# Kernel optimization log

Measured on AMD Instinct MI355X. Metric: run time of the kernel, lower is better.

The kernel has to match this reference:

```python
import jax, jax.numpy as jnp
import numpy as np

NEG_SLOPE = 0.2  # LeakyReLU slope

N, E, D_IN, D_OUT, H, NBIN = 50000, 500000, 256, 256, 8, 10
DH = D_OUT // H


def setup_inputs() -> dict:
    key = jax.random.key(0)
    ks = jax.random.split(key, 9)
    emb_rel = jax.random.normal(ks[0], (N, D_IN), dtype=jnp.float32)
    head_idxs = jax.random.randint(ks[1], (E,), 0, N, dtype=jnp.int32)
    tail_idxs = jax.random.randint(ks[2], (E,), 0, N, dtype=jnp.int32)
    bins = jax.random.randint(ks[3], (E,), 0, NBIN, dtype=jnp.int32)
    # xavier-normal-ish scaled params (gain for relu)
    attn_proj_w = jax.random.normal(ks[4], (D_OUT, 2 * D_IN), dtype=jnp.float32) * (1.4142 * (2.0 / (2 * D_IN + D_OUT)) ** 0.5)
    attn_proj_b = jnp.zeros((D_OUT,), dtype=jnp.float32)
    attn_bin = jax.random.normal(ks[5], (NBIN, H, 1), dtype=jnp.float32) * 0.3
    attn_vec = jax.random.normal(ks[6], (1, H, DH), dtype=jnp.float32) * (1.4142 * (2.0 / (H + DH)) ** 0.5)
    aggr_proj_w = jax.random.normal(ks[7], (D_OUT, D_IN), dtype=jnp.float32) * (1.4142 * (2.0 / (D_IN + D_OUT)) ** 0.5)
    aggr_proj_b = jnp.zeros((D_OUT,), dtype=jnp.float32)
    return {
        "emb_rel": emb_rel,
        "head_idxs": head_idxs,
        "tail_idxs": tail_idxs,
        "bins": bins,
        "attn_proj_w": attn_proj_w,
        "attn_proj_b": attn_proj_b,
        "attn_bin": attn_bin,
        "attn_vec": attn_vec,
        "aggr_proj_w": aggr_proj_w,
        "aggr_proj_b": aggr_proj_b,
        "num_nodes": N,
    }


def reference(emb_rel, head_idxs, tail_idxs, bins, attn_proj_w, attn_proj_b,
              attn_bin, attn_vec, aggr_proj_w, aggr_proj_b, num_nodes):
    num_head, dim_hid = attn_vec.shape[1], attn_vec.shape[2]
    eh = emb_rel[head_idxs]                      # (E, D_in)
    et = emb_rel[tail_idxs]                      # (E, D_in)
    concat = jnp.concatenate([eh, et], axis=-1)  # (E, 2*D_in)
    proj = (concat @ attn_proj_w.T + attn_proj_b).reshape(-1, num_head, dim_hid)
    lrelu = jnp.where(proj >= 0, proj, NEG_SLOPE * proj)
    # raw attention logits per edge/head: (E, H, 1)
    attn_raw = jnp.sum(lrelu * attn_vec, axis=-1, keepdims=True) + attn_bin[bins]
    # segmented softmax over edges grouped by head node
    seg_max = jax.ops.segment_max(attn_raw, head_idxs, num_segments=num_nodes)
    seg_max = jnp.where(jnp.isfinite(seg_max), seg_max, 0.0)  # empty segments -> 0 (never gathered anyway)
    attn_val = jnp.exp(attn_raw - seg_max[head_idxs])
    attn_sums = jax.ops.segment_sum(attn_val, head_idxs, num_segments=num_nodes)
    beta = attn_val / (attn_sums[head_idxs] + 1e-16)            # (E, H, 1)
    aggr = (et @ aggr_proj_w.T + aggr_proj_b).reshape(-1, num_head, dim_hid)
    out = jax.ops.segment_sum(beta * aggr, head_idxs, num_segments=num_nodes)
    return out.reshape(num_nodes, num_head * dim_hid)
```

## Files before the change

kernel.cpp:

```cpp
#include <hip/hip_runtime.h>
#include <math.h>

#define D_IN 256
#define D_OUT 256
#define NH 8
#define DH 32
#define NBIN 10
#define NEG_SLOPE 0.2f
#define CAP 96
#define LOG2E 1.4426950408889634f
#define THR 8.0f

typedef short short4v __attribute__((ext_vector_type(4)));
typedef short short8 __attribute__((ext_vector_type(8)));
typedef float f32x4 __attribute__((ext_vector_type(4)));

__device__ __forceinline__ unsigned short f2bf(float f) {
  unsigned u = __float_as_uint(f);
  unsigned r = u + 0x7fffu + ((u >> 16) & 1u);
  return (unsigned short)(r >> 16);
}
__device__ __forceinline__ float bf2f(unsigned short s) {
  return __uint_as_float((unsigned)s << 16);
}

__device__ __forceinline__ void gload16(const void* g, void* l) {
  __builtin_amdgcn_global_load_lds(
      (const __attribute__((address_space(1))) unsigned int*)g,
      (__attribute__((address_space(3))) unsigned int*)l, 16, 0, 0);
}

__global__ void prep_kernel(const float* __restrict__ attn_w,
                            const float* __restrict__ attn_b,
                            const float* __restrict__ aggr_w,
                            const float* __restrict__ aggr_b,
                            const float* __restrict__ emb,
                            unsigned short* __restrict__ WCbf,
                            float* __restrict__ biasC,
                            unsigned short* __restrict__ embbf,
                            int* __restrict__ cnt, int N) {
  const int b = blockIdx.x, k = threadIdx.x;
  if (b < 768) {
    const int j = b;
    int idx0 = j * 256 + k;
    if (idx0 < N) cnt[idx0] = 0;
    float v, bia = 0.f;
    if (j < 256) {
      v = attn_w[j * 512 + k];
    } else {
      int idx = j - 256, g = idx >> 3, r = idx & 7;
      if (r < 4) { int c = g * 4 + r;     v = attn_w[c * 512 + 256 + k]; bia = attn_b[c]; }
      else       { int c = g * 4 + r - 4; v = aggr_w[c * 256 + k];       bia = aggr_b[c]; }
    }
    WCbf[j * 256 + k] = f2bf(v);
    if (k == 0) biasC[j] = bia;
  } else {
    const long long total = (long long)N * 256;
    long long i = (((long long)(b - 768)) * 256 + k) * 8;
    if (i >= total) return;
    float4 a = *(const float4*)(emb + i);
    float4 c = *(const float4*)(emb + i + 4);
    short8 o;
    o[0] = (short)f2bf(a.x); o[1] = (short)f2bf(a.y);
    o[2] = (short)f2bf(a.z); o[3] = (short)f2bf(a.w);
    o[4] = (short)f2bf(c.x); o[5] = (short)f2bf(c.y);
    o[6] = (short)f2bf(c.z); o[7] = (short)f2bf(c.w);
    *(short8*)(embbf + i) = o;
  }
}

#define EPAD 36
__global__ __launch_bounds__(256) void gemm_bf16_kernel(
    const unsigned short* __restrict__ Abf,
    const unsigned short* __restrict__ Bbf,
    const float* __restrict__ biasC,
    unsigned short* __restrict__ P1bf, unsigned short* __restrict__ P2A, int N) {
  __shared__ char smem[49152];
  float* Ls = (float*)smem;
  const int tid = threadIdx.x;
  const int row0 = blockIdx.x * 128, col0 = blockIdx.y * 256;
  const int wave = tid >> 6, l = tid & 63;
  const int wm = wave >> 1, wn = wave & 1;
  const int lr = l & 15;
  const int lq = l >> 4;
  const int srow = tid >> 2;
  const int sk = (tid & 3) * 8;
  int ar0 = row0 + srow;      if (ar0 >= N) ar0 = N - 1;
  int ar1 = row0 + 64 + srow; if (ar1 >= N) ar1 = N - 1;
  const unsigned short* pa0 = Abf + (size_t)ar0 * 256 + sk;
  const unsigned short* pa1 = Abf + (size_t)ar1 * 256 + sk;
  const unsigned short* pb0 = Bbf + (size_t)(col0 + srow) * 256 + sk;
  const unsigned short* pb1 = Bbf + (size_t)(col0 + 64 + srow) * 256 + sk;
  const unsigned short* pb2 = Bbf + (size_t)(col0 + 128 + srow) * 256 + sk;
  const unsigned short* pb3 = Bbf + (size_t)(col0 + 192 + srow) * 256 + sk;

  auto STAGE = [&](int buf, int kk) {
    unsigned short* base = (unsigned short*)(smem + buf * 24576);
    gload16(pa0 + kk, base + wave * 512);
    gload16(pa1 + kk, base + 2048 + wave * 512);
    gload16(pb0 + kk, base + 4096 + wave * 512);
    gload16(pb1 + kk, base + 6144 + wave * 512);
    gload16(pb2 + kk, base + 8192 + wave * 512);
    gload16(pb3 + kk, base + 10240 + wave * 512);
  };

  f32x4 acc[4][8] = {};
  STAGE(0, 0);
  __syncthreads();
  int cur = 0;
  for (int t = 0; t < 8; ++t) {
    if (t < 7) STAGE(cur ^ 1, (t + 1) * 32);
    __builtin_amdgcn_sched_barrier(0);
    const unsigned short* As = (const unsigned short*)(smem + cur * 24576);
    const unsigned short* Bs = As + 4096;
    short8 af[4], bfr[8];
#pragma unroll
    for (int i = 0; i < 4; ++i)
      af[i] = *(const short8*)&As[(wm * 64 + i * 16 + lr) * 32 + lq * 8];
#pragma unroll
    for (int j = 0; j < 8; ++j)
      bfr[j] = *(const short8*)&Bs[(wn * 128 + j * 16 + lr) * 32 + lq * 8];
#pragma unroll
    for (int i = 0; i < 4; ++i)
#pragma unroll
      for (int j = 0; j < 8; ++j)
        acc[i][j] = __builtin_amdgcn_mfma_f32_16x16x32_bf16(af[i], bfr[j], acc[i][j], 0, 0, 0);
    __syncthreads();
    cur ^= 1;
  }
  for (int j = 0; j < 8; ++j) {
    __syncthreads();
    const float bias = biasC[col0 + wn * 128 + j * 16 + lr];
#pragma unroll
    for (int i = 0; i < 4; ++i) {
      const int lrow = wm * 64 + i * 16 + lq * 4;
#pragma unroll
      for (int r = 0; r < 4; ++r)
        Ls[(lrow + r) * EPAD + wn * 16 + lr] = acc[i][j][r] + bias;
    }
    __syncthreads();
    const int o = tid & 3, half = o >> 1, part = o & 1;
#pragma unroll
    for (int s = 0; s < 2; ++s) {
      const int row = (tid >> 2) + s * 64;
      const int grow = row0 + row;
      if (grow < N) {
        const float* src = &Ls[row * EPAD + half * 16 + part * 8];
        short8 v;
#pragma unroll
        for (int q = 0; q < 8; ++q) v[q] = (short)f2bf(src[q]);
        const int colb = half * 128 + j * 16 + part * 8;
        if (col0 == 0)
          *(short8*)(P1bf + (size_t)grow * 256 + colb) = v;
        else
          *(short8*)(P2A + (size_t)grow * 512 + (col0 - 256) + colb) = v;
      }
    }
  }
}

__global__ void bucket_scatter_kernel(const int* __restrict__ head,
                                      const int* __restrict__ tail,
                                      const int* __restrict__ bins,
                                      int* __restrict__ cnt,
                                      int* __restrict__ bucket, int E) {
  int e = blockIdx.x * blockDim.x + threadIdx.x;
  if (e >= E) return;
  int h = head[e];
  int slot = atomicAdd(&cnt[h], 1);
  if (slot < CAP) bucket[(size_t)h * CAP + slot] = (bins[e] << 16) | tail[e];
}

template <int PAT>
__device__ __forceinline__ float swz_add(float s) {
  return s + __uint_as_float(
      (unsigned)__builtin_amdgcn_ds_swizzle((int)__float_as_uint(s), PAT));
}

__device__ __forceinline__ short8 ldP2A(const unsigned short* __restrict__ P2A,
                                        int t, int l8) {
  return *(const short8*)(P2A + ((size_t)(t & 0xFFFF) << 9) + l8);
}

__device__ __forceinline__ float edge_dot(short8 c, float4 p1, float4 av) {
  float x, s;
  x = p1.x + bf2f((unsigned short)c[0]); s  = fmaxf(x, NEG_SLOPE * x) * av.x;
  x = p1.y + bf2f((unsigned short)c[1]); s += fmaxf(x, NEG_SLOPE * x) * av.y;
  x = p1.z + bf2f((unsigned short)c[2]); s += fmaxf(x, NEG_SLOPE * x) * av.z;
  x = p1.w + bf2f((unsigned short)c[3]); s += fmaxf(x, NEG_SLOPE * x) * av.w;
  s = swz_add<0x041F>(s);
  s = swz_add<0x081F>(s);
  s = swz_add<0x101F>(s);
  return s;
}

__device__ __forceinline__ float4 edge_val(short8 c) {
  float4 v;
  v.x = bf2f((unsigned short)c[4]); v.y = bf2f((unsigned short)c[5]);
  v.z = bf2f((unsigned short)c[6]); v.w = bf2f((unsigned short)c[7]);
  return v;
}

__global__ __launch_bounds__(128) void node_aggr_kernel(
    const unsigned short* __restrict__ P1bf, const unsigned short* __restrict__ P2A,
    const int* __restrict__ cnt, const int* __restrict__ bucket,
    const float* __restrict__ attn_vec, const float* __restrict__ attn_bin,
    float* __restrict__ out, int N) {
  __shared__ float sbin[NBIN * NH];
  const int tid = threadIdx.x;
  if (tid < NBIN * NH) sbin[tid] = attn_bin[tid] * LOG2E;
  __syncthreads();
  const int nu = __builtin_amdgcn_readfirstlane(blockIdx.x * 2 + (tid >> 6));
  if (nu >= N) return;
  const int l = tid & 63;
  const int l8 = l * 8;
  const int h = l >> 3;
  float4 av = *(const float4*)(attn_vec + l * 4);
  av.x *= LOG2E; av.y *= LOG2E; av.z *= LOG2E; av.w *= LOG2E;
  const short4v p1s = *(const short4v*)(P1bf + (size_t)nu * 256 + l * 4);
  float4 p1;
  p1.x = bf2f((unsigned short)p1s[0]); p1.y = bf2f((unsigned short)p1s[1]);
  p1.z = bf2f((unsigned short)p1s[2]); p1.w = bf2f((unsigned short)p1s[3]);
  const int* brow = bucket + (size_t)nu * CAP;
  int d = cnt[nu];
  if (d > CAP) d = CAP;
  float m = 0.f, m8 = 0.f, sum = 0.f;
  float4 acc = make_float4(0.f, 0.f, 0.f, 0.f);
  if (d > 0) {
    const int dm1 = d - 1;
    const int t0 = brow[0];
    short8 c0 = ldP2A(P2A, t0, l8);
    int ta[4];
    short8 ca[4];
#pragma unroll
    for (int k = 0; k < 4; ++k) {
      const int ja = (1 + k <= dm1) ? 1 + k : dm1;
      ta[k] = brow[ja];
      ca[k] = ldP2A(P2A, ta[k], l8);
    }
    __builtin_amdgcn_sched_barrier(0);
    m = edge_dot(c0, p1, av) + sbin[(t0 >> 16) * NH + h];
    m8 = m + THR;
    sum = 1.f;
    const float4 v0 = edge_val(c0);
    acc.x = v0.x; acc.y = v0.y; acc.z = v0.z; acc.w = v0.w;
    int i = 1;
#pragma unroll 2
    for (; i + 3 < d; i += 4) {
      int tn[4];
      short8 cn[4];
#pragma unroll
      for (int k = 0; k < 4; ++k) {
        const int jn = (i + 4 + k <= dm1) ? i + 4 + k : dm1;
        tn[k] = brow[jn];
        cn[k] = ldP2A(P2A, tn[k], l8);
      }
      __builtin_amdgcn_sched_barrier(0);
      float lg[4];
#pragma unroll
      for (int k = 0; k < 4; ++k)
        lg[k] = edge_dot(ca[k], p1, av) + sbin[(ta[k] >> 16) * NH + h];
      const float lmax = fmaxf(fmaxf(lg[0], lg[1]), fmaxf(lg[2], lg[3]));
      if (__any(lmax > m8)) {
        const float mn = fmaxf(m, lmax);
        const float sc = __builtin_amdgcn_exp2f(m - mn);
        sum *= sc; acc.x *= sc; acc.y *= sc; acc.z *= sc; acc.w *= sc;
        m = mn; m8 = mn + THR;
      }
#pragma unroll
      for (int k = 0; k < 4; ++k) {
        const float w = __builtin_amdgcn_exp2f(lg[k] - m);
        const float4 v = edge_val(ca[k]);
        sum += w;
        acc.x += w * v.x; acc.y += w * v.y;
        acc.z += w * v.z; acc.w += w * v.w;
      }
#pragma unroll
      for (int k = 0; k < 4; ++k) { ta[k] = tn[k]; ca[k] = cn[k]; }
    }
    const int r = d - i;
#pragma unroll
    for (int k = 0; k < 3; ++k) {
      if (k < r) {
        const float lgk = edge_dot(ca[k], p1, av) + sbin[(ta[k] >> 16) * NH + h];
        if (__any(lgk > m8)) {
          const float mn = fmaxf(m, lgk);
          const float sc = __builtin_amdgcn_exp2f(m - mn);
          sum *= sc; acc.x *= sc; acc.y *= sc; acc.z *= sc; acc.w *= sc;
          m = mn; m8 = mn + THR;
        }
        const float w = __builtin_amdgcn_exp2f(lgk - m);
        const float4 v = edge_val(ca[k]);
        sum += w;
        acc.x += w * v.x; acc.y += w * v.y;
        acc.z += w * v.z; acc.w += w * v.w;
      }
    }
  }
  const float inv = 1.f / (sum + 1e-16f);
  float4 o;
  o.x = acc.x * inv; o.y = acc.y * inv; o.z = acc.z * inv; o.w = acc.w * inv;
  *(float4*)(out + (size_t)nu * 256 + l * 4) = o;
}

extern "C" void kernel_launch(void* const* d_in, const int* in_sizes, int n_in,
                              void* d_out, int out_size, void* d_ws, size_t ws_size,
                              hipStream_t stream) {
  const float* emb      = (const float*)d_in[0];
  const int*   head     = (const int*)d_in[1];
  const int*   tail     = (const int*)d_in[2];
  const int*   bins     = (const int*)d_in[3];
  const float* attn_w   = (const float*)d_in[4];
  const float* attn_b   = (const float*)d_in[5];
  const float* attn_bin = (const float*)d_in[6];
  const float* attn_vec = (const float*)d_in[7];
  const float* aggr_w   = (const float*)d_in[8];
  const float* aggr_b   = (const float*)d_in[9];
  float* out = (float*)d_out;

  const int N = in_sizes[0] / D_IN;
  const int E = in_sizes[1];

  char* ws = (char*)d_ws;
  size_t off = 0;
  auto walloc = [&](size_t bytes) -> void* {
    void* p = ws + off;
    off += (bytes + 255) & ~(size_t)255;
    return p;
  };
  unsigned short* P1bf   = (unsigned short*)walloc((size_t)N * 256 * sizeof(short));
  unsigned short* P2A    = (unsigned short*)walloc((size_t)N * 512 * sizeof(short));
  unsigned short* embbf  = (unsigned short*)walloc((size_t)N * 256 * sizeof(short));
  unsigned short* WCbf   = (unsigned short*)walloc((size_t)768 * 256 * sizeof(short));
  float*          biasC  = (float*)walloc(768 * sizeof(float));
  int*            cnt    = (int*)walloc((size_t)N * sizeof(int));
  int*            bucket = (int*)walloc((size_t)N * CAP * sizeof(int));

  const int conv_blocks = (int)(((long long)N * 256 / 8 + 255) / 256);
  prep_kernel<<<768 + conv_blocks, 256, 0, stream>>>(attn_w, attn_b, aggr_w, aggr_b,
                                                     emb, WCbf, biasC, embbf, cnt, N);
  prep_kernel<<<768 + conv_blocks, 256, 0, stream>>>(attn_w, attn_b, aggr_w, aggr_b,
                                                     emb, WCbf, biasC, embbf, cnt, N);

  dim3 ggrid((N + 127) / 128, 768 / 256);
  gemm_bf16_kernel<<<ggrid, 256, 0, stream>>>(embbf, WCbf, biasC, P1bf, P2A, N);
  gemm_bf16_kernel<<<ggrid, 256, 0, stream>>>(embbf, WCbf, biasC, P1bf, P2A, N);

  bucket_scatter_kernel<<<(E + 255) / 256, 256, 0, stream>>>(head, tail, bins, cnt, bucket, E);

  node_aggr_kernel<<<(N + 1) / 2, 128, 0, stream>>>(P1bf, P2A, cnt, bucket,
                                                    attn_vec, attn_bin, out, N);
}
```

Baseline: 333.8 us.

## Merge bucket scatter into GEMM launch and drop duplicated prep/GEMM launches

The before code launched prep_kernel and gemm_bf16_kernel twice each, doing redundant work. The new code launches each once and folds the edge bucket-scatter into the same grid as the GEMM, with the first blocks handling edge atomics and the rest doing GEMM tiles. This removes the duplicate launches and lets the scatter overlap with the GEMM instead of running as a separate serialized kernel. Sharing a grid adds some block-index arithmetic and possible contention between atomic-heavy and compute blocks.

```diff
diff --git a/kernel.cpp b/kernel.cpp
--- a/kernel.cpp
+++ b/kernel.cpp
@@ -70,15 +70,29 @@
 }
 
 #define EPAD 36
-__global__ __launch_bounds__(256) void gemm_bf16_kernel(
+__global__ __launch_bounds__(256) void gemm_scatter_kernel(
     const unsigned short* __restrict__ Abf,
     const unsigned short* __restrict__ Bbf,
     const float* __restrict__ biasC,
-    unsigned short* __restrict__ P1bf, unsigned short* __restrict__ P2A, int N) {
+    unsigned short* __restrict__ P1bf, unsigned short* __restrict__ P2A,
+    const int* __restrict__ head, const int* __restrict__ tail,
+    const int* __restrict__ bins, int* __restrict__ cnt,
+    int* __restrict__ bucket, int N, int E, int nscb, int nrt) {
+  const int tid = threadIdx.x;
+  const int b = blockIdx.x;
+  if (b < nscb) {
+    int e = b * 256 + tid;
+    if (e < E) {
+      int h = head[e];
+      int slot = atomicAdd(&cnt[h], 1);
+      if (slot < CAP) bucket[(size_t)h * CAP + slot] = (bins[e] << 16) | tail[e];
+    }
+    return;
+  }
   __shared__ char smem[49152];
   float* Ls = (float*)smem;
-  const int tid = threadIdx.x;
-  const int row0 = blockIdx.x * 128, col0 = blockIdx.y * 256;
+  const int gb = b - nscb;
+  const int row0 = (gb % nrt) * 128, col0 = (gb / nrt) * 256;
   const int wave = tid >> 6, l = tid & 63;
   const int wm = wave >> 1, wn = wave & 1;
   const int lr = l & 15;
@@ -157,18 +171,6 @@
       }
     }
   }
-}
-
-__global__ void bucket_scatter_kernel(const int* __restrict__ head,
-                                      const int* __restrict__ tail,
-                                      const int* __restrict__ bins,
-                                      int* __restrict__ cnt,
-                                      int* __restrict__ bucket, int E) {
-  int e = blockIdx.x * blockDim.x + threadIdx.x;
-  if (e >= E) return;
-  int h = head[e];
-  int slot = atomicAdd(&cnt[h], 1);
-  if (slot < CAP) bucket[(size_t)h * CAP + slot] = (bins[e] << 16) | tail[e];
 }
 
 template <int PAT>
@@ -339,14 +341,12 @@
   const int conv_blocks = (int)(((long long)N * 256 / 8 + 255) / 256);
   prep_kernel<<<768 + conv_blocks, 256, 0, stream>>>(attn_w, attn_b, aggr_w, aggr_b,
                                                      emb, WCbf, biasC, embbf, cnt, N);
-  prep_kernel<<<768 + conv_blocks, 256, 0, stream>>>(attn_w, attn_b, aggr_w, aggr_b,
-                                                     emb, WCbf, biasC, embbf, cnt, N);
-
-  dim3 ggrid((N + 127) / 128, 768 / 256);
-  gemm_bf16_kernel<<<ggrid, 256, 0, stream>>>(embbf, WCbf, biasC, P1bf, P2A, N);
-  gemm_bf16_kernel<<<ggrid, 256, 0, stream>>>(embbf, WCbf, biasC, P1bf, P2A, N);
-
-  bucket_scatter_kernel<<<(E + 255) / 256, 256, 0, stream>>>(head, tail, bins, cnt, bucket, E);
+
+  const int nscb = (E + 255) / 256;
+  const int nrt = (N + 127) / 128;
+  gemm_scatter_kernel<<<nscb + nrt * 3, 256, 0, stream>>>(
+      embbf, WCbf, biasC, P1bf, P2A, head, tail, bins, cnt, bucket,
+      N, E, nscb, nrt);
 
   node_aggr_kernel<<<(N + 1) / 2, 128, 0, stream>>>(P1bf, P2A, cnt, bucket,
                                                     attn_vec, attn_bin, out, N);
```

Result: faster. 267.1 us (-20.0%).
